# Kernel tuning notes

Measured on AMD Instinct MI355X. Metric: run time of the kernel, lower is better.

Reference implementation:

```python
import jax, jax.numpy as jnp
import numpy as np

B, L, E = 4, 1024, 1024
H = 16
HD = E // H
CLIP = 16
SCALE = 1.0 / np.sqrt(HD)


def setup_inputs() -> dict:
    key = jax.random.key(0)
    ks = jax.random.split(key, 13)
    def lin(k, fan_in, fan_out, gain):
        # xavier_uniform
        limit = gain * np.sqrt(6.0 / (fan_in + fan_out))
        return jax.random.uniform(k, (fan_out, fan_in), jnp.float32, -limit, limit)
    inv_sqrt2 = 1.0 / np.sqrt(2.0)
    return {
        "query": jax.random.normal(ks[0], (B, L, E), jnp.float32),
        "key": jax.random.normal(ks[1], (B, L, E), jnp.float32),
        "value": jax.random.normal(ks[2], (B, L, E), jnp.float32),
        "wq": lin(ks[3], E, E, inv_sqrt2), "bq": jnp.zeros((E,), jnp.float32),
        "wk": lin(ks[4], E, E, inv_sqrt2), "bk": jnp.zeros((E,), jnp.float32),
        "wv": lin(ks[5], E, E, inv_sqrt2), "bv": jnp.zeros((E,), jnp.float32),
        "wo": lin(ks[6], E, E, 1.0), "bo": jnp.zeros((E,), jnp.float32),
        "rel_k": jax.random.normal(ks[7], (2 * CLIP + 1, HD), jnp.float32) * 0.02,
        "rel_v": jax.random.normal(ks[8], (2 * CLIP + 1, HD), jnp.float32) * 0.02,
    }


def _heads(x):  # (B, L, E) -> (B, H, L, HD)
    return x.reshape(B, L, H, HD).transpose(0, 2, 1, 3)


def reference(query, key, value, wq, bq, wk, bk, wv, bv, wo, bo, rel_k, rel_v):
    q = _heads(query @ wq.T + bq)
    k = _heads(key @ wk.T + bk)
    v = _heads(value @ wv.T + bv)

    # relative-position index matrix (L_q, L_k), clipped to [-CLIP, CLIP]
    pos = jnp.arange(L)
    dist = jnp.clip(pos[None, :] - pos[:, None], -CLIP, CLIP) + CLIP
    r_k = rel_k[dist]  # (L, L, HD)
    r_v = rel_v[dist]  # (L, L, HD)

    dot = jnp.einsum('bhid,bhjd->bhij', q, k)
    rel = jnp.einsum('bhid,ijd->bhij', q, r_k)
    scores = (dot + rel) * SCALE
    attn = jax.nn.softmax(scores, axis=-1)

    y = jnp.einsum('bhij,bhjd->bhid', attn, v) + jnp.einsum('bhij,ijd->bhid', attn, r_v)
    y = y.transpose(0, 2, 1, 3).reshape(B, L, E)
    return y @ wo.T + bo
```

## Files before the change

kernel.cpp:

```cpp
#include <hip/hip_runtime.h>

#define BB 4
#define LL 1024
#define EE 1024
#define HH 16
#define HD 64
#define NBUCKET 33
#define SCALE 0.125f
#define SC2 (0.125f * 1.44269504088896f)

typedef unsigned short u16;
using f32x4 = __attribute__((ext_vector_type(4))) float;
using s16x8 = __attribute__((ext_vector_type(8))) short;

__device__ __forceinline__ u16 f2bf(float f) {
  union { float f; unsigned u; } x; x.f = f;
  unsigned r = (x.u + 0x7fffu + ((x.u >> 16) & 1u)) >> 16;
  return (u16)r;
}

__device__ __forceinline__ void gld_lds16(const void* g, void* s) {
  __builtin_amdgcn_global_load_lds((const __attribute__((address_space(1))) void*)g,
                                   (__attribute__((address_space(3))) void*)s, 16, 0, 0);
}

__global__ __launch_bounds__(256) void cvt_all(
    const float* __restrict__ q, const float* __restrict__ k, const float* __restrict__ v,
    const float* __restrict__ wq, const float* __restrict__ wk, const float* __restrict__ wv,
    const float* __restrict__ wo, const float* __restrict__ rk,
    u16* __restrict__ oq, u16* __restrict__ ok, u16* __restrict__ ov,
    u16* __restrict__ owq, u16* __restrict__ owk, u16* __restrict__ owv,
    u16* __restrict__ owo, u16* __restrict__ ork) {
  const int bid = blockIdx.x;
  const int tid = threadIdx.x;
  if (bid < 12288) {
    const int z = bid >> 12;
    const int i = (bid & 4095) * 256 + tid;
    const float* in = z == 0 ? q : (z == 1 ? k : v);
    u16* out = z == 0 ? oq : (z == 1 ? ok : ov);
    float4 f = ((const float4*)in)[i];
    ushort4 o;
    o.x = f2bf(f.x); o.y = f2bf(f.y); o.z = f2bf(f.z); o.w = f2bf(f.w);
    ((ushort4*)out)[i] = o;
  } else if (bid < 16384) {
    const int z = (bid - 12288) >> 10;
    const int i = ((bid - 12288) & 1023) * 256 + tid;
    const float* in = z == 0 ? wq : (z == 1 ? wk : (z == 2 ? wv : wo));
    u16* out = z == 0 ? owq : (z == 1 ? owk : (z == 2 ? owv : owo));
    float4 f = ((const float4*)in)[i];
    ushort4 o;
    o.x = f2bf(f.x); o.y = f2bf(f.y); o.z = f2bf(f.z); o.w = f2bf(f.w);
    ((ushort4*)out)[i] = o;
  } else {
    const int i = (bid - 16384) * 256 + tid;
    ork[i] = (i < 33 * 64) ? f2bf(rk[i]) : (u16)0;
  }
}

template <int MODE>
__device__ __forceinline__ void gemm128_bt(const u16* __restrict__ A,
                                           const u16* __restrict__ Bw,
                                           const float* __restrict__ bias,
                                           u16* __restrict__ obf,
                                           float* __restrict__ ofp,
                                           int M, int N, int K, int m0, int n0) {
  __shared__ u16 a_sm[128 * 64];
  __shared__ u16 b_sm[128 * 64];
  const int tid = threadIdx.x;
  const int wave = tid >> 6, lane = tid & 63;
  const int row16 = lane & 15, quad = lane >> 4;
  const int wr = (wave >> 1) * 64, wc = (wave & 1) * 64;
  const int srow = lane >> 3, scol = (lane & 7) * 8;

  f32x4 acc[4][4] = {};

  for (int k0 = 0; k0 < K; k0 += 64) {
#pragma unroll
    for (int t = 0; t < 4; ++t) {
      const int chunk = wave * 4 + t;
      const int r = chunk * 8 + srow;
      gld_lds16(A + (size_t)(m0 + r) * K + k0 + scol, a_sm + chunk * 512);
      gld_lds16(Bw + (size_t)(n0 + r) * K + k0 + scol, b_sm + chunk * 512);
    }
    __syncthreads();
#pragma unroll
    for (int ks = 0; ks < 2; ++ks) {
      s16x8 af[4], bf[4];
#pragma unroll
      for (int mi = 0; mi < 4; ++mi)
        af[mi] = *(const s16x8*)&a_sm[(wr + mi * 16 + row16) * 64 + ks * 32 + quad * 8];
#pragma unroll
      for (int ni = 0; ni < 4; ++ni)
        bf[ni] = *(const s16x8*)&b_sm[(wc + ni * 16 + row16) * 64 + ks * 32 + quad * 8];
#pragma unroll
      for (int mi = 0; mi < 4; ++mi)
#pragma unroll
        for (int ni = 0; ni < 4; ++ni)
          acc[mi][ni] = __builtin_amdgcn_mfma_f32_16x16x32_bf16(af[mi], bf[ni], acc[mi][ni], 0, 0, 0);
    }
    __syncthreads();
  }

#pragma unroll
  for (int mi = 0; mi < 4; ++mi)
#pragma unroll
    for (int ni = 0; ni < 4; ++ni) {
      const int n = n0 + wc + ni * 16 + row16;
      const float bn = bias[n];
      if (MODE == 2) {
        const int mr0 = m0 + wr + mi * 16 + quad * 4;
        const int b = mr0 >> 10, l = mr0 & 1023;
        const int h = n >> 6, hd = n & 63;
        ushort4 o;
        o.x = f2bf(acc[mi][ni][0] + bn);
        o.y = f2bf(acc[mi][ni][1] + bn);
        o.z = f2bf(acc[mi][ni][2] + bn);
        o.w = f2bf(acc[mi][ni][3] + bn);
        *(ushort4*)&obf[((size_t)((b * HH + h) * HD + hd)) * LL + l] = o;
      } else {
#pragma unroll
        for (int r = 0; r < 4; ++r) {
          const int m = m0 + wr + mi * 16 + quad * 4 + r;
          const float v = acc[mi][ni][r] + bn;
          if (MODE == 0) {
            const int b = m >> 10, l = m & 1023, h = n >> 6, hd = n & 63;
            obf[((size_t)((b * HH + h) * LL + l)) * HD + hd] = f2bf(v);
          } else {
            ofp[(size_t)m * N + n] = v;
          }
        }
      }
    }
}

__global__ __launch_bounds__(256) void proj_gemm(
    const u16* __restrict__ xq, const u16* __restrict__ xk, const u16* __restrict__ xv,
    const u16* __restrict__ wqb, const u16* __restrict__ wkb, const u16* __restrict__ wvb,
    const float* __restrict__ bq, const float* __restrict__ bk, const float* __restrict__ bv,
    u16* __restrict__ oq, u16* __restrict__ ok, u16* __restrict__ ovt) {
  if (blockIdx.z == 0)
    gemm128_bt<0>(xq, wqb, bq, oq, nullptr, BB * LL, EE, EE, blockIdx.y * 128, blockIdx.x * 128);
  else if (blockIdx.z == 1)
    gemm128_bt<0>(xk, wkb, bk, ok, nullptr, BB * LL, EE, EE, blockIdx.y * 128, blockIdx.x * 128);
  else
    gemm128_bt<2>(xv, wvb, bv, ovt, nullptr, BB * LL, EE, EE, blockIdx.y * 128, blockIdx.x * 128);
}

__global__ __launch_bounds__(256) void out_gemm(const u16* __restrict__ Y,
                                                const u16* __restrict__ wob,
                                                const float* __restrict__ bo,
                                                float* __restrict__ out) {
  gemm128_bt<1>(Y, wob, bo, nullptr, out, BB * LL, EE, EE, blockIdx.y * 128, blockIdx.x * 128);
}

__global__ __launch_bounds__(256) void attn_fused(
    const u16* __restrict__ Q, const u16* __restrict__ Kb, const u16* __restrict__ Vt,
    const u16* __restrict__ RKp, const float* __restrict__ RV, u16* __restrict__ Y) {
  __shared__ __align__(16) float qr_sm[4][576];
  __shared__ __align__(16) float s_sm[4][16 * 36];
  __shared__ __align__(16) unsigned char kv[16384];

  const int tid = threadIdx.x;
  const int wave = tid >> 6, lane = tid & 63;
  const int row16 = lane & 15, quad = lane >> 4;
  const int bh = blockIdx.x & 63;
  const int i0 = (blockIdx.x >> 6) * 64;
  const int wq0 = i0 + wave * 16;
  const u16* qp = Q + (size_t)bh * LL * HD;
  const char* kpB = (const char*)(Kb + (size_t)bh * LL * HD);
  const char* vpB = (const char*)(Vt + (size_t)bh * HD * LL);

  float* qr_w = &qr_sm[wave][0];
  float* s_w = &s_sm[wave][0];

  int srcK[2], srcV[2];
#pragma unroll
  for (int t = 0; t < 2; ++t) {
    const int cK = (wave * 2 + t) * 64 + lane;
    const int rw = cK >> 3;
    const int cb = ((cK * 16) & 127) ^ ((rw & 7) << 4);
    srcK[t] = rw * 128 + cb;
    srcV[t] = rw * 2048 + cb;
  }
  const int q2 = row16 >> 2;
  const int prow = ((((q2 << 1) | (q2 >> 1)) & 3) << 2) + (row16 & 3);
  const int swzK = (prow & 7) << 4;
  const int swzV = (row16 & 7) << 4;
  const int rho4 = (((quad << 1) | (quad >> 1)) & 3) << 2;

#pragma unroll
  for (int t = 0; t < 2; ++t) {
    gld_lds16(kpB + srcK[t], kv + (wave * 2 + t) * 1024);
    gld_lds16(vpB + srcV[t], kv + 8192 + (wave * 2 + t) * 1024);
  }

  for (int t = lane; t < 16 * 36; t += 64) s_w[t] = 0.f;

  s16x8 qf[2];
#pragma unroll
  for (int ks = 0; ks < 2; ++ks)
    qf[ks] = *(const s16x8*)(qp + (size_t)(wq0 + row16) * HD + ks * 32 + quad * 8);

  f32x4 a0, a2;
#pragma unroll
  for (int nt = 0; nt < 3; ++nt) {
    f32x4 a = {};
#pragma unroll
    for (int ks = 0; ks < 2; ++ks) {
      s16x8 afr = *(const s16x8*)(RKp + (size_t)(nt * 16 + row16) * HD + ks * 32 + quad * 8);
      a = __builtin_amdgcn_mfma_f32_16x16x32_bf16(afr, qf[ks], a, 0, 0, 0);
    }
    if (nt == 0) a0 = a;
    if (nt == 2) a2 = a;
#pragma unroll
    for (int r = 0; r < 4; ++r) {
      const int bk = nt * 16 + quad * 4 + r;
      if (bk < NBUCKET) qr_w[bk * 17 + row16] = a[r];
    }
  }
  const float blo = __shfl(a0[0], row16);
  const float bhi = __shfl(a2[0], row16);

  f32x4 oacc[4] = {};
  float rsum = 0.f, plos = 0.f, phis = 0.f;
  int baseg[4];
#pragma unroll
  for (int g = 0; g < 4; ++g) baseg[g] = g * 16 + rho4 - wq0 - row16;

  for (int jt = 0; jt < 16; ++jt) {
    const int j0 = jt * 64;
    if (jt) {
#pragma unroll
      for (int t = 0; t < 2; ++t) {
        gld_lds16(kpB + (size_t)j0 * 128 + srcK[t], kv + (wave * 2 + t) * 1024);
        gld_lds16(vpB + (size_t)j0 * 2 + srcV[t], kv + 8192 + (wave * 2 + t) * 1024);
      }
    }
    asm volatile("s_waitcnt vmcnt(0)" ::: "memory");
    __builtin_amdgcn_s_barrier();
    __builtin_amdgcn_sched_barrier(0);

    f32x4 sacc[4] = {};
#pragma unroll
    for (int ks = 0; ks < 2; ++ks)
#pragma unroll
      for (int g = 0; g < 4; ++g) {
        const int L = (g * 16 + prow) * 128 + ks * 64 + quad * 16;
        const s16x8 kfr = *(const s16x8*)(kv + (L ^ swzK));
        sacc[g] = __builtin_amdgcn_mfma_f32_16x16x32_bf16(kfr, qf[ks], sacc[g], 0, 0, 0);
      }

    unsigned pk[4][2];
    const bool far_lo = (wq0 >= j0 + 79);
    const bool far_hi = (j0 >= wq0 + 31);
    if (far_lo || far_hi) {
      const float bb = (far_lo ? blo : bhi) * SC2;
      float tacc = 0.f;
#pragma unroll
      for (int g = 0; g < 4; ++g)
#pragma unroll
        for (int rr = 0; rr < 2; ++rr) {
          const float pv0 = __builtin_amdgcn_exp2f(sacc[g][rr * 2] * SC2 + bb);
          const float pv1 = __builtin_amdgcn_exp2f(sacc[g][rr * 2 + 1] * SC2 + bb);
          tacc += pv0 + pv1;
          unsigned c;
          asm("v_cvt_pk_bf16_f32 %0, %1, %2" : "=v"(c) : "v"(pv0), "v"(pv1));
          pk[g][rr] = c;
        }
      rsum += tacc;
      if (far_lo) plos += tacc; else phis += tacc;
    } else {
#pragma unroll
      for (int g = 0; g < 4; ++g)
#pragma unroll
        for (int rr = 0; rr < 2; ++rr) {
          float pv2[2];
#pragma unroll
          for (int e = 0; e < 2; ++e) {
            const int r = rr * 2 + e;
            const int dr = baseg[g] + j0 + r;
            int bk = dr < -16 ? -16 : (dr > 16 ? 16 : dr);
            bk += 16;
            const float bias = qr_w[bk * 17 + row16];
            const float pv = __builtin_amdgcn_exp2f((sacc[g][r] + bias) * SC2);
            pv2[e] = pv;
            rsum += pv;
            if (dr <= -16) plos += pv;
            else if (dr >= 16) phis += pv;
            else atomicAdd(&s_w[row16 * 36 + bk], pv);
          }
          unsigned c;
          asm("v_cvt_pk_bf16_f32 %0, %1, %2" : "=v"(c) : "v"(pv2[0]), "v"(pv2[1]));
          pk[g][rr] = c;
        }
    }

    s16x8 pf[2];
#pragma unroll
    for (int ks = 0; ks < 2; ++ks) {
      unsigned x0 = pk[ks * 2][0], y0 = pk[ks * 2 + 1][0];
      unsigned x1 = pk[ks * 2][1], y1 = pk[ks * 2 + 1][1];
      asm("v_permlane32_swap_b32 %0, %1" : "+v"(x0), "+v"(y0));
      asm("v_permlane32_swap_b32 %0, %1" : "+v"(x1), "+v"(y1));
      union { unsigned u[4]; s16x8 v; } pfu;
      pfu.u[0] = x0; pfu.u[1] = x1; pfu.u[2] = y0; pfu.u[3] = y1;
      pf[ks] = pfu.v;
    }

#pragma unroll
    for (int ks = 0; ks < 2; ++ks)
#pragma unroll
      for (int dt = 0; dt < 4; ++dt) {
        const int L = (dt * 16 + row16) * 128 + ks * 64 + quad * 16;
        const s16x8 vfr = *(const s16x8*)(kv + 8192 + (L ^ swzV));
        oacc[dt] = __builtin_amdgcn_mfma_f32_16x16x32_bf16(vfr, pf[ks], oacc[dt], 0, 0, 0);
      }

    asm volatile("s_waitcnt lgkmcnt(0)" ::: "memory");
    __builtin_amdgcn_s_barrier();
    __builtin_amdgcn_sched_barrier(0);
  }

  float t1 = rsum + __shfl_xor(rsum, 16);
  const float lacc = t1 + __shfl_xor(t1, 32);
  t1 = plos + __shfl_xor(plos, 16);
  const float slo = t1 + __shfl_xor(t1, 32);
  t1 = phis + __shfl_xor(phis, 16);
  const float shi = t1 + __shfl_xor(t1, 32);

  float* rv_sm = (float*)kv;
  for (int t = tid; t < NBUCKET * HD; t += 256) rv_sm[t] = RV[t];
  __syncthreads();

  const int b = bh >> 4, h = bh & 15;
  float rel[4][4] = {};
  for (int bk = 0; bk < NBUCKET; ++bk) {
    float sv = s_w[row16 * 36 + bk];
    if (bk == 0) sv += slo;
    if (bk == 32) sv += shi;
#pragma unroll
    for (int dt = 0; dt < 4; ++dt) {
      const f32x4 rv4 = *(const f32x4*)&rv_sm[bk * HD + dt * 16 + quad * 4];
#pragma unroll
      for (int r = 0; r < 4; ++r) rel[dt][r] += sv * rv4[r];
    }
  }
  const float inv = 1.0f / lacc;
#pragma unroll
  for (int dt = 0; dt < 4; ++dt) {
    ushort4 o;
    o.x = f2bf((oacc[dt][0] + rel[dt][0]) * inv);
    o.y = f2bf((oacc[dt][1] + rel[dt][1]) * inv);
    o.z = f2bf((oacc[dt][2] + rel[dt][2]) * inv);
    o.w = f2bf((oacc[dt][3] + rel[dt][3]) * inv);
    *(ushort4*)&Y[((size_t)(b * LL + wq0 + row16)) * EE + h * HD + dt * 16 + quad * 4] = o;
  }
}

extern "C" void kernel_launch(void* const* d_in, const int* in_sizes, int n_in,
                              void* d_out, int out_size, void* d_ws, size_t ws_size,
                              hipStream_t stream) {
  const float* query = (const float*)d_in[0];
  const float* key_  = (const float*)d_in[1];
  const float* value = (const float*)d_in[2];
  const float* wq = (const float*)d_in[3];
  const float* bq = (const float*)d_in[4];
  const float* wk = (const float*)d_in[5];
  const float* bk = (const float*)d_in[6];
  const float* wv = (const float*)d_in[7];
  const float* bv = (const float*)d_in[8];
  const float* wo = (const float*)d_in[9];
  const float* bo = (const float*)d_in[10];
  const float* rel_k = (const float*)d_in[11];
  const float* rel_v = (const float*)d_in[12];

  char* base = (char*)d_ws;
  size_t off = 0;
  auto alloc = [&](size_t bytes) -> void* {
    void* p = base + off;
    off += (bytes + 255) & ~(size_t)255;
    return p;
  };
  const size_t XE = (size_t)BB * LL * EE;
  u16* xq    = (u16*)alloc(XE * 2);
  u16* xk    = (u16*)alloc(XE * 2);
  u16* xv    = (u16*)alloc(XE * 2);
  u16* wqb   = (u16*)alloc((size_t)EE * EE * 2);
  u16* wkb   = (u16*)alloc((size_t)EE * EE * 2);
  u16* wvb   = (u16*)alloc((size_t)EE * EE * 2);
  u16* wob   = (u16*)alloc((size_t)EE * EE * 2);
  u16* q_ws  = (u16*)alloc(XE * 2);
  u16* k_ws  = (u16*)alloc(XE * 2);
  u16* vt_ws = (u16*)alloc(XE * 2);
  u16* relkp = (u16*)alloc(48 * 64 * 2);
  u16* y_ws = xq;

  cvt_all<<<16396, 256, 0, stream>>>(query, key_, value, wq, wk, wv, wo, rel_k,
                                     xq, xk, xv, wqb, wkb, wvb, wob, relkp);

  proj_gemm<<<dim3(EE / 128, BB * LL / 128, 3), 256, 0, stream>>>(
      xq, xk, xv, wqb, wkb, wvb, bq, bk, bv, q_ws, k_ws, vt_ws);

  attn_fused<<<1024, 256, 0, stream>>>(q_ws, k_ws, vt_ws, relkp, rel_v, y_ws);

  out_gemm<<<dim3(EE / 128, BB * LL / 128), 256, 0, stream>>>(y_ws, wob, bo, (float*)d_out);
}
```

Measured before the change: 250.7 us.

## Process two query tiles per wave and double-buffer K/V in attention kernel

Each attention block now covers 128 query rows instead of 64: every wave handles two 16-row query tiles that share each loaded K/V fragment. K/V tiles are double-buffered in LDS, so the next tile's global-to-LDS load is issued before computing on the current one. This halves the attention grid and K/V traffic per query row and aims to hide load latency. In exchange it raises register and LDS use per block, and leaves fewer blocks to spread across CUs.

```diff
diff --git a/kernel.cpp b/kernel.cpp
--- a/kernel.cpp
+++ b/kernel.cpp
@@ -153,25 +153,90 @@
   gemm128_bt<1>(Y, wob, bo, nullptr, out, BB * LL, EE, EE, blockIdx.y * 128, blockIdx.x * 128);
 }
 
+__device__ __forceinline__ void softmax_pack(
+    const f32x4 sacc[4], int j0, int wq0, float blo, float bhi,
+    const float* qr_w, float* s_w, const int baseg[4], int row16,
+    float& rsum, float& plos, float& phis, unsigned pk[4][2]) {
+  const bool far_lo = (wq0 >= j0 + 79);
+  const bool far_hi = (j0 >= wq0 + 31);
+  if (far_lo || far_hi) {
+    const float bb = (far_lo ? blo : bhi) * SC2;
+    float tacc = 0.f;
+#pragma unroll
+    for (int g = 0; g < 4; ++g)
+#pragma unroll
+      for (int rr = 0; rr < 2; ++rr) {
+        const float pv0 = __builtin_amdgcn_exp2f(sacc[g][rr * 2] * SC2 + bb);
+        const float pv1 = __builtin_amdgcn_exp2f(sacc[g][rr * 2 + 1] * SC2 + bb);
+        tacc += pv0 + pv1;
+        unsigned c;
+        asm("v_cvt_pk_bf16_f32 %0, %1, %2" : "=v"(c) : "v"(pv0), "v"(pv1));
+        pk[g][rr] = c;
+      }
+    rsum += tacc;
+    if (far_lo) plos += tacc; else phis += tacc;
+  } else {
+#pragma unroll
+    for (int g = 0; g < 4; ++g)
+#pragma unroll
+      for (int rr = 0; rr < 2; ++rr) {
+        float pv2[2];
+#pragma unroll
+        for (int e = 0; e < 2; ++e) {
+          const int r = rr * 2 + e;
+          const int dr = baseg[g] + j0 + r;
+          int bk = dr < -16 ? -16 : (dr > 16 ? 16 : dr);
+          bk += 16;
+          const float bias = qr_w[bk * 17 + row16];
+          const float pv = __builtin_amdgcn_exp2f((sacc[g][r] + bias) * SC2);
+          pv2[e] = pv;
+          rsum += pv;
+          if (dr <= -16) plos += pv;
+          else if (dr >= 16) phis += pv;
+          else atomicAdd(&s_w[row16 * 36 + bk], pv);
+        }
+        unsigned c;
+        asm("v_cvt_pk_bf16_f32 %0, %1, %2" : "=v"(c) : "v"(pv2[0]), "v"(pv2[1]));
+        pk[g][rr] = c;
+      }
+  }
+}
+
+__device__ __forceinline__ void pf_assemble(const unsigned pk[4][2], s16x8 pf[2]) {
+#pragma unroll
+  for (int ks = 0; ks < 2; ++ks) {
+    unsigned x0 = pk[ks * 2][0], y0 = pk[ks * 2 + 1][0];
+    unsigned x1 = pk[ks * 2][1], y1 = pk[ks * 2 + 1][1];
+    asm("v_permlane32_swap_b32 %0, %1" : "+v"(x0), "+v"(y0));
+    asm("v_permlane32_swap_b32 %0, %1" : "+v"(x1), "+v"(y1));
+    union { unsigned u[4]; s16x8 v; } pfu;
+    pfu.u[0] = x0; pfu.u[1] = x1; pfu.u[2] = y0; pfu.u[3] = y1;
+    pf[ks] = pfu.v;
+  }
+}
+
 __global__ __launch_bounds__(256) void attn_fused(
     const u16* __restrict__ Q, const u16* __restrict__ Kb, const u16* __restrict__ Vt,
     const u16* __restrict__ RKp, const float* __restrict__ RV, u16* __restrict__ Y) {
-  __shared__ __align__(16) float qr_sm[4][576];
-  __shared__ __align__(16) float s_sm[4][16 * 36];
-  __shared__ __align__(16) unsigned char kv[16384];
+  __shared__ __align__(16) float qr_sm[4][2][576];
+  __shared__ __align__(16) float s_sm[4][2][576];
+  __shared__ __align__(16) unsigned char kv[2][16384];
 
   const int tid = threadIdx.x;
   const int wave = tid >> 6, lane = tid & 63;
   const int row16 = lane & 15, quad = lane >> 4;
   const int bh = blockIdx.x & 63;
-  const int i0 = (blockIdx.x >> 6) * 64;
-  const int wq0 = i0 + wave * 16;
+  const int i0 = (blockIdx.x >> 6) * 128;
+  const int wq0a = i0 + wave * 16;
+  const int wq0b = wq0a + 64;
   const u16* qp = Q + (size_t)bh * LL * HD;
   const char* kpB = (const char*)(Kb + (size_t)bh * LL * HD);
   const char* vpB = (const char*)(Vt + (size_t)bh * HD * LL);
 
-  float* qr_w = &qr_sm[wave][0];
-  float* s_w = &s_sm[wave][0];
+  float* qr_wa = &qr_sm[wave][0][0];
+  float* qr_wb = &qr_sm[wave][1][0];
+  float* s_wa = &s_sm[wave][0][0];
+  float* s_wb = &s_sm[wave][1][0];
 
   int srcK[2], srcV[2];
 #pragma unroll
@@ -190,170 +255,152 @@
 
 #pragma unroll
   for (int t = 0; t < 2; ++t) {
-    gld_lds16(kpB + srcK[t], kv + (wave * 2 + t) * 1024);
-    gld_lds16(vpB + srcV[t], kv + 8192 + (wave * 2 + t) * 1024);
-  }
-
-  for (int t = lane; t < 16 * 36; t += 64) s_w[t] = 0.f;
-
-  s16x8 qf[2];
-#pragma unroll
-  for (int ks = 0; ks < 2; ++ks)
-    qf[ks] = *(const s16x8*)(qp + (size_t)(wq0 + row16) * HD + ks * 32 + quad * 8);
-
-  f32x4 a0, a2;
+    gld_lds16(kpB + srcK[t], kv[0] + (wave * 2 + t) * 1024);
+    gld_lds16(vpB + srcV[t], kv[0] + 8192 + (wave * 2 + t) * 1024);
+  }
+
+  for (int t = lane; t < 1152; t += 64) s_wa[t] = 0.f;
+
+  s16x8 qfa[2], qfb[2];
+#pragma unroll
+  for (int ks = 0; ks < 2; ++ks) {
+    qfa[ks] = *(const s16x8*)(qp + (size_t)(wq0a + row16) * HD + ks * 32 + quad * 8);
+    qfb[ks] = *(const s16x8*)(qp + (size_t)(wq0b + row16) * HD + ks * 32 + quad * 8);
+  }
+
+  f32x4 a0a, a2a, a0b, a2b;
 #pragma unroll
   for (int nt = 0; nt < 3; ++nt) {
-    f32x4 a = {};
+    f32x4 aa = {}, ab = {};
 #pragma unroll
     for (int ks = 0; ks < 2; ++ks) {
       s16x8 afr = *(const s16x8*)(RKp + (size_t)(nt * 16 + row16) * HD + ks * 32 + quad * 8);
-      a = __builtin_amdgcn_mfma_f32_16x16x32_bf16(afr, qf[ks], a, 0, 0, 0);
-    }
-    if (nt == 0) a0 = a;
-    if (nt == 2) a2 = a;
+      aa = __builtin_amdgcn_mfma_f32_16x16x32_bf16(afr, qfa[ks], aa, 0, 0, 0);
+      ab = __builtin_amdgcn_mfma_f32_16x16x32_bf16(afr, qfb[ks], ab, 0, 0, 0);
+    }
+    if (nt == 0) { a0a = aa; a0b = ab; }
+    if (nt == 2) { a2a = aa; a2b = ab; }
 #pragma unroll
     for (int r = 0; r < 4; ++r) {
       const int bk = nt * 16 + quad * 4 + r;
-      if (bk < NBUCKET) qr_w[bk * 17 + row16] = a[r];
-    }
-  }
-  const float blo = __shfl(a0[0], row16);
-  const float bhi = __shfl(a2[0], row16);
-
-  f32x4 oacc[4] = {};
-  float rsum = 0.f, plos = 0.f, phis = 0.f;
-  int baseg[4];
-#pragma unroll
-  for (int g = 0; g < 4; ++g) baseg[g] = g * 16 + rho4 - wq0 - row16;
+      if (bk < NBUCKET) {
+        qr_wa[bk * 17 + row16] = aa[r];
+        qr_wb[bk * 17 + row16] = ab[r];
+      }
+    }
+  }
+  const float bloa = __shfl(a0a[0], row16);
+  const float bhia = __shfl(a2a[0], row16);
+  const float blob = __shfl(a0b[0], row16);
+  const float bhib = __shfl(a2b[0], row16);
+
+  f32x4 oa[4] = {}, ob[4] = {};
+  float rsuma = 0.f, plosa = 0.f, phisa = 0.f;
+  float rsumb = 0.f, plosb = 0.f, phisb = 0.f;
+  int basega[4], basegb[4];
+#pragma unroll
+  for (int g = 0; g < 4; ++g) {
+    basega[g] = g * 16 + rho4 - wq0a - row16;
+    basegb[g] = basega[g] - 64;
+  }
+
+  asm volatile("s_waitcnt vmcnt(0) lgkmcnt(0)" ::: "memory");
+  __builtin_amdgcn_s_barrier();
+  __builtin_amdgcn_sched_barrier(0);
 
   for (int jt = 0; jt < 16; ++jt) {
     const int j0 = jt * 64;
-    if (jt) {
+    const unsigned char* cur = kv[jt & 1];
+
+    if (jt < 15) {
+      unsigned char* nxt = (unsigned char*)kv[(jt + 1) & 1];
+      const size_t j1 = (size_t)(j0 + 64);
 #pragma unroll
       for (int t = 0; t < 2; ++t) {
-        gld_lds16(kpB + (size_t)j0 * 128 + srcK[t], kv + (wave * 2 + t) * 1024);
-        gld_lds16(vpB + (size_t)j0 * 2 + srcV[t], kv + 8192 + (wave * 2 + t) * 1024);
-      }
-    }
-    asm volatile("s_waitcnt vmcnt(0)" ::: "memory");
+        gld_lds16(kpB + j1 * 128 + srcK[t], nxt + (wave * 2 + t) * 1024);
+        gld_lds16(vpB + j1 * 2 + srcV[t], nxt + 8192 + (wave * 2 + t) * 1024);
+      }
+    }
+
+    f32x4 sa[4] = {}, sb[4] = {};
+#pragma unroll
+    for (int ks = 0; ks < 2; ++ks)
+#pragma unroll
+      for (int g = 0; g < 4; ++g) {
+        const int L = (g * 16 + prow) * 128 + ks * 64 + quad * 16;
+        const s16x8 kfr = *(const s16x8*)(cur + (L ^ swzK));
+        sa[g] = __builtin_amdgcn_mfma_f32_16x16x32_bf16(kfr, qfa[ks], sa[g], 0, 0, 0);
+        sb[g] = __builtin_amdgcn_mfma_f32_16x16x32_bf16(kfr, qfb[ks], sb[g], 0, 0, 0);
+      }
+
+    unsigned pka[4][2], pkb[4][2];
+    softmax_pack(sa, j0, wq0a, bloa, bhia, qr_wa, s_wa, basega, row16,
+                 rsuma, plosa, phisa, pka);
+    softmax_pack(sb, j0, wq0b, blob, bhib, qr_wb, s_wb, basegb, row16,
+                 rsumb, plosb, phisb, pkb);
+
+    s16x8 pfa[2], pfb[2];
+    pf_assemble(pka, pfa);
+    pf_assemble(pkb, pfb);
+
+#pragma unroll
+    for (int ks = 0; ks < 2; ++ks)
+#pragma unroll
+      for (int dt = 0; dt < 4; ++dt) {
+        const int L = (dt * 16 + row16) * 128 + ks * 64 + quad * 16;
+        const s16x8 vfr = *(const s16x8*)(cur + 8192 + (L ^ swzV));
+        oa[dt] = __builtin_amdgcn_mfma_f32_16x16x32_bf16(vfr, pfa[ks], oa[dt], 0, 0, 0);
+        ob[dt] = __builtin_amdgcn_mfma_f32_16x16x32_bf16(vfr, pfb[ks], ob[dt], 0, 0, 0);
+      }
+
+    asm volatile("s_waitcnt vmcnt(0) lgkmcnt(0)" ::: "memory");
     __builtin_amdgcn_s_barrier();
     __builtin_amdgcn_sched_barrier(0);
-
-    f32x4 sacc[4] = {};
-#pragma unroll
-    for (int ks = 0; ks < 2; ++ks)
-#pragma unroll
-      for (int g = 0; g < 4; ++g) {
-        const int L = (g * 16 + prow) * 128 + ks * 64 + quad * 16;
-        const s16x8 kfr = *(const s16x8*)(kv + (L ^ swzK));
-        sacc[g] = __builtin_amdgcn_mfma_f32_16x16x32_bf16(kfr, qf[ks], sacc[g], 0, 0, 0);
-      }
-
-    unsigned pk[4][2];
-    const bool far_lo = (wq0 >= j0 + 79);
-    const bool far_hi = (j0 >= wq0 + 31);
-    if (far_lo || far_hi) {
-      const float bb = (far_lo ? blo : bhi) * SC2;
-      float tacc = 0.f;
-#pragma unroll
-      for (int g = 0; g < 4; ++g)
-#pragma unroll
-        for (int rr = 0; rr < 2; ++rr) {
-          const float pv0 = __builtin_amdgcn_exp2f(sacc[g][rr * 2] * SC2 + bb);
-          const float pv1 = __builtin_amdgcn_exp2f(sacc[g][rr * 2 + 1] * SC2 + bb);
-          tacc += pv0 + pv1;
-          unsigned c;
-          asm("v_cvt_pk_bf16_f32 %0, %1, %2" : "=v"(c) : "v"(pv0), "v"(pv1));
-          pk[g][rr] = c;
-        }
-      rsum += tacc;
-      if (far_lo) plos += tacc; else phis += tacc;
-    } else {
-#pragma unroll
-      for (int g = 0; g < 4; ++g)
-#pragma unroll
-        for (int rr = 0; rr < 2; ++rr) {
-          float pv2[2];
-#pragma unroll
-          for (int e = 0; e < 2; ++e) {
-            const int r = rr * 2 + e;
-            const int dr = baseg[g] + j0 + r;
-            int bk = dr < -16 ? -16 : (dr > 16 ? 16 : dr);
-            bk += 16;
-            const float bias = qr_w[bk * 17 + row16];
-            const float pv = __builtin_amdgcn_exp2f((sacc[g][r] + bias) * SC2);
-            pv2[e] = pv;
-            rsum += pv;
-            if (dr <= -16) plos += pv;
-            else if (dr >= 16) phis += pv;
-            else atomicAdd(&s_w[row16 * 36 + bk], pv);
-          }
-          unsigned c;
-          asm("v_cvt_pk_bf16_f32 %0, %1, %2" : "=v"(c) : "v"(pv2[0]), "v"(pv2[1]));
-          pk[g][rr] = c;
-        }
-    }
-
-    s16x8 pf[2];
-#pragma unroll
-    for (int ks = 0; ks < 2; ++ks) {
-      unsigned x0 = pk[ks * 2][0], y0 = pk[ks * 2 + 1][0];
-      unsigned x1 = pk[ks * 2][1], y1 = pk[ks * 2 + 1][1];
-      asm("v_permlane32_swap_b32 %0, %1" : "+v"(x0), "+v"(y0));
-      asm("v_permlane32_swap_b32 %0, %1" : "+v"(x1), "+v"(y1));
-      union { unsigned u[4]; s16x8 v; } pfu;
-      pfu.u[0] = x0; pfu.u[1] = x1; pfu.u[2] = y0; pfu.u[3] = y1;
-      pf[ks] = pfu.v;
-    }
-
-#pragma unroll
-    for (int ks = 0; ks < 2; ++ks)
-#pragma unroll
-      for (int dt = 0; dt < 4; ++dt) {
-        const int L = (dt * 16 + row16) * 128 + ks * 64 + quad * 16;
-        const s16x8 vfr = *(const s16x8*)(kv + 8192 + (L ^ swzV));
-        oacc[dt] = __builtin_amdgcn_mfma_f32_16x16x32_bf16(vfr, pf[ks], oacc[dt], 0, 0, 0);
-      }
-
-    asm volatile("s_waitcnt lgkmcnt(0)" ::: "memory");
-    __builtin_amdgcn_s_barrier();
-    __builtin_amdgcn_sched_barrier(0);
-  }
-
-  float t1 = rsum + __shfl_xor(rsum, 16);
-  const float lacc = t1 + __shfl_xor(t1, 32);
-  t1 = plos + __shfl_xor(plos, 16);
-  const float slo = t1 + __shfl_xor(t1, 32);
-  t1 = phis + __shfl_xor(phis, 16);
-  const float shi = t1 + __shfl_xor(t1, 32);
+  }
+
+  float t1;
+  t1 = rsuma + __shfl_xor(rsuma, 16); const float lacca = t1 + __shfl_xor(t1, 32);
+  t1 = plosa + __shfl_xor(plosa, 16); const float sloa = t1 + __shfl_xor(t1, 32);
+  t1 = phisa + __shfl_xor(phisa, 16); const float shia = t1 + __shfl_xor(t1, 32);
+  t1 = rsumb + __shfl_xor(rsumb, 16); const float laccb = t1 + __shfl_xor(t1, 32);
+  t1 = plosb + __shfl_xor(plosb, 16); const float slob = t1 + __shfl_xor(t1, 32);
+  t1 = phisb + __shfl_xor(phisb, 16); const float shib = t1 + __shfl_xor(t1, 32);
 
   float* rv_sm = (float*)kv;
   for (int t = tid; t < NBUCKET * HD; t += 256) rv_sm[t] = RV[t];
   __syncthreads();
 
   const int b = bh >> 4, h = bh & 15;
-  float rel[4][4] = {};
-  for (int bk = 0; bk < NBUCKET; ++bk) {
-    float sv = s_w[row16 * 36 + bk];
-    if (bk == 0) sv += slo;
-    if (bk == 32) sv += shi;
+#pragma unroll
+  for (int tile = 0; tile < 2; ++tile) {
+    const float* s_w = tile == 0 ? s_wa : s_wb;
+    const float slo = tile == 0 ? sloa : slob;
+    const float shi = tile == 0 ? shia : shib;
+    const float lacc = tile == 0 ? lacca : laccb;
+    const f32x4* oacc = tile == 0 ? oa : ob;
+    const int wq0 = tile == 0 ? wq0a : wq0b;
+    float rel[4][4] = {};
+    for (int bk = 0; bk < NBUCKET; ++bk) {
+      float sv = s_w[row16 * 36 + bk];
+      if (bk == 0) sv += slo;
+      if (bk == 32) sv += shi;
+#pragma unroll
+      for (int dt = 0; dt < 4; ++dt) {
+        const f32x4 rv4 = *(const f32x4*)&rv_sm[bk * HD + dt * 16 + quad * 4];
+#pragma unroll
+        for (int r = 0; r < 4; ++r) rel[dt][r] += sv * rv4[r];
+      }
+    }
+    const float inv = 1.0f / lacc;
 #pragma unroll
     for (int dt = 0; dt < 4; ++dt) {
-      const f32x4 rv4 = *(const f32x4*)&rv_sm[bk * HD + dt * 16 + quad * 4];
-#pragma unroll
-      for (int r = 0; r < 4; ++r) rel[dt][r] += sv * rv4[r];
-    }
-  }
-  const float inv = 1.0f / lacc;
-#pragma unroll
-  for (int dt = 0; dt < 4; ++dt) {
-    ushort4 o;
-    o.x = f2bf((oacc[dt][0] + rel[dt][0]) * inv);
-    o.y = f2bf((oacc[dt][1] + rel[dt][1]) * inv);
-    o.z = f2bf((oacc[dt][2] + rel[dt][2]) * inv);
-    o.w = f2bf((oacc[dt][3] + rel[dt][3]) * inv);
-    *(ushort4*)&Y[((size_t)(b * LL + wq0 + row16)) * EE + h * HD + dt * 16 + quad * 4] = o;
+      ushort4 o;
+      o.x = f2bf((oacc[dt][0] + rel[dt][0]) * inv);
+      o.y = f2bf((oacc[dt][1] + rel[dt][1]) * inv);
+      o.z = f2bf((oacc[dt][2] + rel[dt][2]) * inv);
+      o.w = f2bf((oacc[dt][3] + rel[dt][3]) * inv);
+      *(ushort4*)&Y[((size_t)(b * LL + wq0 + row16)) * EE + h * HD + dt * 16 + quad * 4] = o;
+    }
   }
 }
 
@@ -401,7 +448,7 @@
   proj_gemm<<<dim3(EE / 128, BB * LL / 128, 3), 256, 0, stream>>>(
       xq, xk, xv, wqb, wkb, wvb, bq, bk, bv, q_ws, k_ws, vt_ws);
 
-  attn_fused<<<1024, 256, 0, stream>>>(q_ws, k_ws, vt_ws, relkp, rel_v, y_ws);
+  attn_fused<<<512, 256, 0, stream>>>(q_ws, k_ws, vt_ws, relkp, rel_v, y_ws);
 
   out_gemm<<<dim3(EE / 128, BB * LL / 128), 256, 0, stream>>>(y_ws, wob, bo, (float*)d_out);
 }
```

Result: slower. 273.1 us (+9.0%).

## Double-buffer GEMM LDS tiles with XOR swizzle and XCD-aware block remapping

Applied to the files above, without the earlier changes.

Both projection and output GEMMs now use a double-buffered LDS pipeline, so the global-to-LDS load of the next K tile overlaps the MFMA work on the current tile. The LDS columns are XOR-swizzled to avoid bank conflicts on the fragment reads. Block indices are remapped so that consecutive work tiles land on the same XCD, which is meant to improve L2 reuse. LDS use per block doubles to 64 KB, which can lower occupancy, and the wait on vmcnt(0) at the end of each iteration limits how much of the load latency is hidden.

```diff
diff --git a/kernel.cpp b/kernel.cpp
--- a/kernel.cpp
+++ b/kernel.cpp
@@ -58,47 +58,65 @@
 }
 
 template <int MODE>
-__device__ __forceinline__ void gemm128_bt(const u16* __restrict__ A,
-                                           const u16* __restrict__ Bw,
-                                           const float* __restrict__ bias,
-                                           u16* __restrict__ obf,
-                                           float* __restrict__ ofp,
-                                           int M, int N, int K, int m0, int n0) {
-  __shared__ u16 a_sm[128 * 64];
-  __shared__ u16 b_sm[128 * 64];
+__device__ __forceinline__ void gemm128_dbuf(u16* __restrict__ sm,
+                                             const u16* __restrict__ A,
+                                             const u16* __restrict__ Bw,
+                                             const float* __restrict__ bias,
+                                             u16* __restrict__ obf,
+                                             float* __restrict__ ofp,
+                                             int N, int K, int m0, int n0) {
   const int tid = threadIdx.x;
   const int wave = tid >> 6, lane = tid & 63;
   const int row16 = lane & 15, quad = lane >> 4;
   const int wr = (wave >> 1) * 64, wc = (wave & 1) * 64;
   const int srow = lane >> 3, scol = (lane & 7) * 8;
+  const int rsw = (row16 & 7) * 8;
 
   f32x4 acc[4][4] = {};
 
-  for (int k0 = 0; k0 < K; k0 += 64) {
+  auto stage = [&](int k0, u16* as, u16* bs) {
 #pragma unroll
     for (int t = 0; t < 4; ++t) {
       const int chunk = wave * 4 + t;
       const int r = chunk * 8 + srow;
-      gld_lds16(A + (size_t)(m0 + r) * K + k0 + scol, a_sm + chunk * 512);
-      gld_lds16(Bw + (size_t)(n0 + r) * K + k0 + scol, b_sm + chunk * 512);
-    }
-    __syncthreads();
+      const int cs = scol ^ ((r & 7) * 8);
+      gld_lds16(A + (size_t)(m0 + r) * K + k0 + cs, as + chunk * 512);
+      gld_lds16(Bw + (size_t)(n0 + r) * K + k0 + cs, bs + chunk * 512);
+    }
+  };
+
+  stage(0, sm, sm + 8192);
+  asm volatile("s_waitcnt vmcnt(0)" ::: "memory");
+  __builtin_amdgcn_s_barrier();
+  __builtin_amdgcn_sched_barrier(0);
+
+  const int NK = K >> 6;
+  for (int kt = 0; kt < NK; ++kt) {
+    u16* as = sm + (kt & 1) * 16384;
+    u16* bs = as + 8192;
+    if (kt + 1 < NK) {
+      u16* an = sm + ((kt + 1) & 1) * 16384;
+      stage((kt + 1) << 6, an, an + 8192);
+    }
 #pragma unroll
     for (int ks = 0; ks < 2; ++ks) {
+      const int cfs = (ks * 32 + quad * 8) ^ rsw;
       s16x8 af[4], bf[4];
 #pragma unroll
       for (int mi = 0; mi < 4; ++mi)
-        af[mi] = *(const s16x8*)&a_sm[(wr + mi * 16 + row16) * 64 + ks * 32 + quad * 8];
+        af[mi] = *(const s16x8*)&as[(wr + mi * 16 + row16) * 64 + cfs];
 #pragma unroll
       for (int ni = 0; ni < 4; ++ni)
-        bf[ni] = *(const s16x8*)&b_sm[(wc + ni * 16 + row16) * 64 + ks * 32 + quad * 8];
+        bf[ni] = *(const s16x8*)&bs[(wc + ni * 16 + row16) * 64 + cfs];
 #pragma unroll
       for (int mi = 0; mi < 4; ++mi)
 #pragma unroll
         for (int ni = 0; ni < 4; ++ni)
           acc[mi][ni] = __builtin_amdgcn_mfma_f32_16x16x32_bf16(af[mi], bf[ni], acc[mi][ni], 0, 0, 0);
     }
-    __syncthreads();
+    asm volatile("s_waitcnt vmcnt(0) lgkmcnt(0)" ::: "memory");
+    __builtin_amdgcn_s_barrier();
+    __builtin_amdgcn_sched_barrier(0);
   }
 
 #pragma unroll
@@ -117,17 +135,19 @@
         o.z = f2bf(acc[mi][ni][2] + bn);
         o.w = f2bf(acc[mi][ni][3] + bn);
         *(ushort4*)&obf[((size_t)((b * HH + h) * HD + hd)) * LL + l] = o;
-      } else {
+      } else if (MODE == 0) {
 #pragma unroll
         for (int r = 0; r < 4; ++r) {
           const int m = m0 + wr + mi * 16 + quad * 4 + r;
           const float v = acc[mi][ni][r] + bn;
-          if (MODE == 0) {
-            const int b = m >> 10, l = m & 1023, h = n >> 6, hd = n & 63;
-            obf[((size_t)((b * HH + h) * LL + l)) * HD + hd] = f2bf(v);
-          } else {
-            ofp[(size_t)m * N + n] = v;
-          }
+          const int b = m >> 10, l = m & 1023, h = n >> 6, hd = n & 63;
+          obf[((size_t)((b * HH + h) * LL + l)) * HD + hd] = f2bf(v);
+        }
+      } else {
+#pragma unroll
+        for (int r = 0; r < 4; ++r) {
+          const int m = m0 + wr + mi * 16 + quad * 4 + r;
+          ofp[(size_t)m * N + n] = acc[mi][ni][r] + bn;
         }
       }
     }
@@ -138,19 +158,28 @@
     const u16* __restrict__ wqb, const u16* __restrict__ wkb, const u16* __restrict__ wvb,
     const float* __restrict__ bq, const float* __restrict__ bk, const float* __restrict__ bv,
     u16* __restrict__ oq, u16* __restrict__ ok, u16* __restrict__ ovt) {
-  if (blockIdx.z == 0)
-    gemm128_bt<0>(xq, wqb, bq, oq, nullptr, BB * LL, EE, EE, blockIdx.y * 128, blockIdx.x * 128);
-  else if (blockIdx.z == 1)
-    gemm128_bt<0>(xk, wkb, bk, ok, nullptr, BB * LL, EE, EE, blockIdx.y * 128, blockIdx.x * 128);
+  __shared__ u16 sm[4 * 8192];
+  const int work = (blockIdx.x & 7) * 96 + (blockIdx.x >> 3);
+  const int z = work >> 8;
+  const int m0 = ((work & 255) >> 3) * 128;
+  const int n0 = (work & 7) * 128;
+  if (z == 0)
+    gemm128_dbuf<0>(sm, xq, wqb, bq, oq, nullptr, EE, EE, m0, n0);
+  else if (z == 1)
+    gemm128_dbuf<0>(sm, xk, wkb, bk, ok, nullptr, EE, EE, m0, n0);
   else
-    gemm128_bt<2>(xv, wvb, bv, ovt, nullptr, BB * LL, EE, EE, blockIdx.y * 128, blockIdx.x * 128);
+    gemm128_dbuf<2>(sm, xv, wvb, bv, ovt, nullptr, EE, EE, m0, n0);
 }
 
 __global__ __launch_bounds__(256) void out_gemm(const u16* __restrict__ Y,
                                                 const u16* __restrict__ wob,
                                                 const float* __restrict__ bo,
                                                 float* __restrict__ out) {
-  gemm128_bt<1>(Y, wob, bo, nullptr, out, BB * LL, EE, EE, blockIdx.y * 128, blockIdx.x * 128);
+  __shared__ u16 sm[4 * 8192];
+  const int work = (blockIdx.x & 7) * 32 + (blockIdx.x >> 3);
+  const int m0 = (work >> 3) * 128;
+  const int n0 = (work & 7) * 128;
+  gemm128_dbuf<1>(sm, Y, wob, bo, nullptr, out, EE, EE, m0, n0);
 }
 
 __global__ __launch_bounds__(256) void attn_fused(
@@ -398,10 +427,10 @@
   cvt_all<<<16396, 256, 0, stream>>>(query, key_, value, wq, wk, wv, wo, rel_k,
                                      xq, xk, xv, wqb, wkb, wvb, wob, relkp);
 
-  proj_gemm<<<dim3(EE / 128, BB * LL / 128, 3), 256, 0, stream>>>(
+  proj_gemm<<<768, 256, 0, stream>>>(
       xq, xk, xv, wqb, wkb, wvb, bq, bk, bv, q_ws, k_ws, vt_ws);
 
   attn_fused<<<1024, 256, 0, stream>>>(q_ws, k_ws, vt_ws, relkp, rel_v, y_ws);
 
-  out_gemm<<<dim3(EE / 128, BB * LL / 128), 256, 0, stream>>>(y_ws, wob, bo, (float*)d_out);
-}
+  out_gemm<<<256, 256, 0, stream>>>(y_ws, wob, bo, (float*)d_out);
+}
```

After: 225.7 us. 10.0% less time.
